# Optimization experiments

Measured on AMD Instinct MI355X. Metric: run time of the kernel, lower is better.

The kernel has to match this reference:

```python
import jax, jax.numpy as jnp
import numpy as np

B, T, D, H = 4, 1024, 1024, 16
DH = D // H
EPS = 1e-5


def setup_inputs() -> dict:
    key = jax.random.key(0)
    ks = jax.random.split(key, 14)
    sc = 1.0 / np.sqrt(D)
    x = jax.random.normal(ks[0], (B, T, D), jnp.float32)
    W_r = jax.random.normal(ks[1], (D, D), jnp.float32) * sc
    W_k = jax.random.normal(ks[2], (D, D), jnp.float32) * sc
    W_v = jax.random.normal(ks[3], (D, D), jnp.float32) * sc
    W_w = jax.random.normal(ks[4], (D, D), jnp.float32) * sc
    W_o = jax.random.normal(ks[5], (D, D), jnp.float32) * sc
    u = jax.random.normal(ks[6], (H, DH), jnp.float32) * 0.1
    tm_r = jax.random.uniform(ks[7], (D,), jnp.float32)
    tm_k = jax.random.uniform(ks[8], (D,), jnp.float32)
    tm_v = jax.random.uniform(ks[9], (D,), jnp.float32)
    tm_w = jax.random.uniform(ks[10], (D,), jnp.float32)
    ln_w = jnp.ones((DH,), jnp.float32) + 0.1 * jax.random.normal(ks[11], (DH,), jnp.float32)
    ln_b = 0.1 * jax.random.normal(ks[12], (DH,), jnp.float32)
    return {"x": x, "W_r": W_r, "W_k": W_k, "W_v": W_v, "W_w": W_w, "W_o": W_o,
            "u": u, "tm_r": tm_r, "tm_k": tm_k, "tm_v": tm_v, "tm_w": tm_w,
            "ln_w": ln_w, "ln_b": ln_b}


def _rwkv6(x, W_r, W_k, W_v, W_w, W_o, u, tm_r, tm_k, tm_v, tm_w, ln_w, ln_b):
    b, t, d = x.shape
    # token-shift mix
    x_prev = jnp.concatenate([jnp.zeros_like(x[:, :1]), x[:, :-1]], axis=1)
    xr = tm_r * x + (1.0 - tm_r) * x_prev
    xk = tm_k * x + (1.0 - tm_k) * x_prev
    xv = tm_v * x + (1.0 - tm_v) * x_prev
    xw = tm_w * x + (1.0 - tm_w) * x_prev
    r = jax.nn.sigmoid(xr @ W_r.T)          # (B,T,D)
    k = xk @ W_k.T
    v = xv @ W_v.T
    w = -jax.nn.softplus(-(xw @ W_w.T)) - 1e-4  # always < 0 -> exp(w) in (0,1)
    r = r.reshape(b, t, H, DH)
    k = k.reshape(b, t, H, DH)
    v = v.reshape(b, t, H, DH)
    w = w.reshape(b, t, H, DH)

    def step(s, rkvw):
        r_t, k_t, v_t, w_t = rkvw  # each (B,H,DH)
        bonus = jnp.exp(u + k_t)[..., :, None] * v_t[..., None, :]  # (B,H,DH,DH)
        o_t = jnp.einsum('bhi,bhij->bhj', r_t, s + bonus)
        s = jnp.exp(w_t)[..., None] * s + k_t[..., :, None] * v_t[..., None, :]
        return s, o_t

    s0 = jnp.zeros((b, H, DH, DH), x.dtype)
    rkvw = tuple(a.transpose(1, 0, 2, 3) for a in (r, k, v, w))  # (T,B,H,DH)
    _, o = jax.lax.scan(step, s0, rkvw)      # o: (T,B,H,DH)
    o = o.transpose(1, 0, 2, 3)              # (B,T,H,DH)
    # group LayerNorm over head dim
    mu = jnp.mean(o, axis=-1, keepdims=True)
    var = jnp.var(o, axis=-1, keepdims=True)
    o = (o - mu) * jax.lax.rsqrt(var + EPS) * ln_w + ln_b
    o = o * r
    return (o.reshape(b, t, d)) @ W_o.T


def reference(x, W_r, W_k, W_v, W_w, W_o, u, tm_r, tm_k, tm_v, tm_w, ln_w, ln_b):
    return _rwkv6(x, W_r, W_k, W_v, W_w, W_o, u, tm_r, tm_k, tm_v, tm_w, ln_w, ln_b)
```

## Files before the change

### kernel.cpp

```cpp
#include <hip/hip_runtime.h>


typedef unsigned short u16;
typedef unsigned int   u32;

typedef __attribute__((ext_vector_type(8))) __bf16 bf16x8;
typedef __attribute__((ext_vector_type(4))) float   f32x4;

#define MB (1u << 20)

#define LDS_PTR(p) ((__attribute__((address_space(3))) void*)(p))
#define GLB_PTR(p) ((const __attribute__((address_space(1))) void*)(p))

__device__ __forceinline__ u16 f2bf(float f) {
  u32 u = __builtin_bit_cast(u32, f);
  u += 0x7FFFu + ((u >> 16) & 1u);
  return (u16)(u >> 16);
}
__device__ __forceinline__ float bf2f(u16 x) {
  u32 u = ((u32)x) << 16;
  return __builtin_bit_cast(float, u);
}
__device__ __forceinline__ u32 pack2(float a, float b) {
  return (u32)f2bf(a) | ((u32)f2bf(b) << 16);
}

__global__ __launch_bounds__(256) void prep_w(
    const float* __restrict__ w0, const float* __restrict__ w1,
    const float* __restrict__ w2, const float* __restrict__ w3,
    const float* __restrict__ w4, u32* __restrict__ out) {
  int idx = blockIdx.x * 256 + threadIdx.x;
  int m = idx >> 19;
  int l = idx & 524287;
  const float* src = (m == 0) ? w0 : (m == 1) ? w1 : (m == 2) ? w2 : (m == 3) ? w3 : w4;
  float2 v = *(const float2*)(src + (size_t)l * 2);
  out[idx] = pack2(v.x, v.y);
}

__global__ __launch_bounds__(256) void prep_mix(
    const float* __restrict__ x,
    const float* __restrict__ tmr, const float* __restrict__ tmk,
    const float* __restrict__ tmv, const float* __restrict__ tmw,
    u32* __restrict__ xr, u32* __restrict__ xk,
    u32* __restrict__ xv, u32* __restrict__ xw) {
  int idx = blockIdx.x * 256 + threadIdx.x;
  int t  = (idx >> 9) & 1023;
  int d0 = (idx & 511) * 2;
  size_t e = (size_t)idx * 2;
  float2 xc = *(const float2*)(x + e);
  float2 xp = make_float2(0.f, 0.f);
  if (t > 0) xp = *(const float2*)(x + e - 1024);
  float2 tm;
  tm = *(const float2*)(tmr + d0);
  xr[idx] = pack2(tm.x * xc.x + (1.f - tm.x) * xp.x, tm.y * xc.y + (1.f - tm.y) * xp.y);
  tm = *(const float2*)(tmk + d0);
  xk[idx] = pack2(tm.x * xc.x + (1.f - tm.x) * xp.x, tm.y * xc.y + (1.f - tm.y) * xp.y);
  tm = *(const float2*)(tmv + d0);
  xv[idx] = pack2(tm.x * xc.x + (1.f - tm.x) * xp.x, tm.y * xc.y + (1.f - tm.y) * xp.y);
  tm = *(const float2*)(tmw + d0);
  xw[idx] = pack2(tm.x * xc.x + (1.f - tm.x) * xp.x, tm.y * xc.y + (1.f - tm.y) * xp.y);
}

__global__ __launch_bounds__(512, 1) void gemm_proj(
    const u16* __restrict__ xr, const u16* __restrict__ xk,
    const u16* __restrict__ xv, const u16* __restrict__ xw,
    const u16* __restrict__ Wr, const u16* __restrict__ Wk,
    const u16* __restrict__ Wv, const u16* __restrict__ Ww,
    u16* __restrict__ rO, u16* __restrict__ kO,
    u16* __restrict__ vO, float* __restrict__ wO) {
  constexpr int KITER = 32;
  constexpr int LDK   = 1024;
  __shared__ __align__(16) u16 Asm[2 * 8192];
  __shared__ __align__(16) u16 Bsm[2 * 8192];

  int mat = blockIdx.z;
  const u16* A = (mat == 0) ? xr : (mat == 1) ? xk : (mat == 2) ? xv : xw;
  const u16* W = (mat == 0) ? Wr : (mat == 1) ? Wk : (mat == 2) ? Wv : Ww;

  int tid = threadIdx.x;
  int m0 = blockIdx.x * 256, n0 = blockIdx.y * 256;
  int wave = tid >> 6, lane = tid & 63;
  int wm = (wave >> 2) * 128;
  int wn = (wave & 3) * 64;
  int r16 = lane & 15, quad = lane >> 4;

  f32x4 acc[8][4] = {};

  int srow0 = wave * 32 + (lane >> 2);
  int srow1 = srow0 + 16;
  int c4    = lane & 3;
  int q0 = c4 ^ ((srow0 >> 1) & 3);
  int q1 = c4 ^ ((srow1 >> 1) & 3);
  const u16* Ag0 = A + (size_t)(m0 + srow0) * LDK + q0 * 8;
  const u16* Ag1 = A + (size_t)(m0 + srow1) * LDK + q1 * 8;
  const u16* Bg0 = W + (size_t)(n0 + srow0) * LDK + q0 * 8;
  const u16* Bg1 = W + (size_t)(n0 + srow1) * LDK + q1 * 8;
  int ldsOff0 = wave * 1024;
  int ldsOff1 = wave * 1024 + 512;

  int aoff[8], boff[4];
#pragma unroll
  for (int mt = 0; mt < 8; ++mt) {
    int r = wm + mt * 16 + r16;
    aoff[mt] = r * 32 + (quad ^ ((r >> 1) & 3)) * 8;
  }
#pragma unroll
  for (int nt = 0; nt < 4; ++nt) {
    int r = wn + nt * 16 + r16;
    boff[nt] = r * 32 + (quad ^ ((r >> 1) & 3)) * 8;
  }

#define ISSUE_TILE(t, buf)                                                              \
  do {                                                                                  \
    int _o = (buf) * 8192, _k = (t) * 32;                                               \
    __builtin_amdgcn_global_load_lds(GLB_PTR(Ag0 + _k), LDS_PTR(Asm + _o + ldsOff0), 16, 0, 0); \
    __builtin_amdgcn_global_load_lds(GLB_PTR(Ag1 + _k), LDS_PTR(Asm + _o + ldsOff1), 16, 0, 0); \
    __builtin_amdgcn_global_load_lds(GLB_PTR(Bg0 + _k), LDS_PTR(Bsm + _o + ldsOff0), 16, 0, 0); \
    __builtin_amdgcn_global_load_lds(GLB_PTR(Bg1 + _k), LDS_PTR(Bsm + _o + ldsOff1), 16, 0, 0); \
  } while (0)

  ISSUE_TILE(0, 0);
  ISSUE_TILE(1, 1);

  int cur = 0;
  for (int i = 0; i < KITER; ++i) {
    if (i < KITER - 1) asm volatile("s_waitcnt vmcnt(4)" ::: "memory");
    else               asm volatile("s_waitcnt vmcnt(0)" ::: "memory");
    __builtin_amdgcn_s_barrier();

    const u16* As = Asm + cur * 8192;
    const u16* Bs = Bsm + cur * 8192;
    bf16x8 af[8], bfm[4];
#pragma unroll
    for (int mt = 0; mt < 8; ++mt) af[mt] = *(const bf16x8*)&As[aoff[mt]];
#pragma unroll
    for (int nt = 0; nt < 4; ++nt) bfm[nt] = *(const bf16x8*)&Bs[boff[nt]];
#pragma unroll
    for (int mt = 0; mt < 8; ++mt)
#pragma unroll
      for (int nt = 0; nt < 4; ++nt)
        acc[mt][nt] = __builtin_amdgcn_mfma_f32_16x16x32_bf16(af[mt], bfm[nt], acc[mt][nt], 0, 0, 0);

    asm volatile("s_waitcnt lgkmcnt(0)" ::: "memory");
    __builtin_amdgcn_s_barrier();
    if (i + 2 < KITER) ISSUE_TILE(i + 2, cur);
    cur ^= 1;
  }
#undef ISSUE_TILE

#pragma unroll
  for (int mt = 0; mt < 8; ++mt) {
#pragma unroll
    for (int nt = 0; nt < 4; ++nt) {
#pragma unroll
      for (int rg = 0; rg < 4; ++rg) {
        int row = m0 + wm + mt * 16 + quad * 4 + rg;
        int col = n0 + wn + nt * 16 + r16;
        float v = acc[mt][nt][rg];
        size_t idx = (size_t)row * 1024 + col;
        if (mat == 0)      rO[idx] = f2bf(1.f / (1.f + __expf(-v)));
        else if (mat == 1) kO[idx] = f2bf(v);
        else if (mat == 2) vO[idx] = f2bf(v);
        else               wO[idx] = v;
      }
    }
  }
}

template <int KITER>
__device__ __forceinline__ void gemm_core(
    const u16* __restrict__ A, const u16* __restrict__ W, float* __restrict__ O,
    u16* Asm, u16* Bsm) {
  constexpr int LDK = KITER * 32;
  int tid = threadIdx.x;
  int m0 = blockIdx.x * 128, n0 = blockIdx.y * 128;
  int wave = tid >> 6, lane = tid & 63;
  int wm = (wave >> 1) * 64, wn = (wave & 1) * 64;
  int r16 = lane & 15, quad = lane >> 4;

  f32x4 acc[4][4] = {};

  int srow0 = wave * 32 + (lane >> 2);
  int srow1 = srow0 + 16;
  int c4    = lane & 3;
  int q0 = c4 ^ ((srow0 >> 1) & 3);
  int q1 = c4 ^ ((srow1 >> 1) & 3);
  const u16* Ag0 = A + (size_t)(m0 + srow0) * LDK + q0 * 8;
  const u16* Ag1 = A + (size_t)(m0 + srow1) * LDK + q1 * 8;
  const u16* Bg0 = W + (size_t)(n0 + srow0) * LDK + q0 * 8;
  const u16* Bg1 = W + (size_t)(n0 + srow1) * LDK + q1 * 8;
  int ldsOff0 = wave * 1024;
  int ldsOff1 = wave * 1024 + 512;

  int aoff[4], boff[4];
#pragma unroll
  for (int mt = 0; mt < 4; ++mt) {
    int r = wm + mt * 16 + r16;
    aoff[mt] = r * 32 + (quad ^ ((r >> 1) & 3)) * 8;
  }
#pragma unroll
  for (int nt = 0; nt < 4; ++nt) {
    int r = wn + nt * 16 + r16;
    boff[nt] = r * 32 + (quad ^ ((r >> 1) & 3)) * 8;
  }

#define ISSUE_TILE(t, buf)                                                              \
  do {                                                                                  \
    int _o = (buf) * 4096, _k = (t) * 32;                                               \
    __builtin_amdgcn_global_load_lds(GLB_PTR(Ag0 + _k), LDS_PTR(Asm + _o + ldsOff0), 16, 0, 0); \
    __builtin_amdgcn_global_load_lds(GLB_PTR(Ag1 + _k), LDS_PTR(Asm + _o + ldsOff1), 16, 0, 0); \
    __builtin_amdgcn_global_load_lds(GLB_PTR(Bg0 + _k), LDS_PTR(Bsm + _o + ldsOff0), 16, 0, 0); \
    __builtin_amdgcn_global_load_lds(GLB_PTR(Bg1 + _k), LDS_PTR(Bsm + _o + ldsOff1), 16, 0, 0); \
  } while (0)

  ISSUE_TILE(0, 0);
  ISSUE_TILE(1, 1);
  ISSUE_TILE(2, 2);

  int cur = 0;
  for (int i = 0; i < KITER; ++i) {
    if (i < KITER - 2)       asm volatile("s_waitcnt vmcnt(8)" ::: "memory");
    else if (i == KITER - 2) asm volatile("s_waitcnt vmcnt(4)" ::: "memory");
    else                     asm volatile("s_waitcnt vmcnt(0)" ::: "memory");
    __builtin_amdgcn_s_barrier();

    const u16* As = Asm + cur * 4096;
    const u16* Bs = Bsm + cur * 4096;
    bf16x8 af[4], bfm[4];
#pragma unroll
    for (int mt = 0; mt < 4; ++mt) af[mt] = *(const bf16x8*)&As[aoff[mt]];
#pragma unroll
    for (int nt = 0; nt < 4; ++nt) bfm[nt] = *(const bf16x8*)&Bs[boff[nt]];
#pragma unroll
    for (int mt = 0; mt < 4; ++mt)
#pragma unroll
      for (int nt = 0; nt < 4; ++nt)
        acc[mt][nt] = __builtin_amdgcn_mfma_f32_16x16x32_bf16(af[mt], bfm[nt], acc[mt][nt], 0, 0, 0);

    asm volatile("s_waitcnt lgkmcnt(0)" ::: "memory");
    __builtin_amdgcn_s_barrier();
    if (i + 3 < KITER) ISSUE_TILE(i + 3, cur);
    cur = (cur == 2) ? 0 : cur + 1;
  }
#undef ISSUE_TILE

#pragma unroll
  for (int mt = 0; mt < 4; ++mt)
#pragma unroll
    for (int nt = 0; nt < 4; ++nt)
#pragma unroll
      for (int rg = 0; rg < 4; ++rg) {
        int row = m0 + wm + mt * 16 + quad * 4 + rg;
        int col = n0 + wn + nt * 16 + r16;
        O[(size_t)row * 1024 + col] = acc[mt][nt][rg];
      }
}

__global__ __launch_bounds__(256) void gemm_out(
    const u16* __restrict__ A, const u16* __restrict__ W, float* __restrict__ O) {
  __shared__ __align__(16) u16 Asm[3 * 4096];
  __shared__ __align__(16) u16 Bsm[3 * 4096];
  gemm_core<32>(A, W, O, Asm, Bsm);
}

__global__ __launch_bounds__(256) void scan_intra(
    const u16* __restrict__ rb, const u16* __restrict__ kb,
    const u16* __restrict__ vb, const float* __restrict__ wb,
    const float* __restrict__ u,
    float* __restrict__ o, u16* __restrict__ rd,
    float* __restrict__ U, float* __restrict__ Dc) {
  int c = blockIdx.x, bh = blockIdx.y;
  int b = bh >> 4, h = bh & 15;
  int tid = threadIdx.x, ig = tid >> 6, j = tid & 63;

  __shared__ __align__(16) float4 combo[4][64];
  __shared__ float vs_[4][64];
  __shared__ float part[4][4][64];

  const float EW_SCALE = 0.99990001f;

  float s[16];
#pragma unroll
  for (int ii = 0; ii < 16; ++ii) s[ii] = 0.f;

  size_t base = ((size_t)(b * 1024 + c * 64)) * 1024 + h * 64 + j;
  float dloc = 1.0f;
  float uval = (ig == 1) ? u[h * 64 + j] : 0.f;

#pragma unroll
  for (int p = 0; p < 2; ++p) {
    size_t idx = base + (size_t)p * 1024;
    if (ig == 0)      combo[p][j].x = bf2f(rb[idx]);
    else if (ig == 1) { float kv = bf2f(kb[idx]); combo[p][j].y = kv; combo[p][j].z = __expf(uval + kv); }
    else if (ig == 2) vs_[p][j] = bf2f(vb[idx]);
    else              combo[p][j].w = EW_SCALE / (1.f + __expf(-wb[idx]));
  }
  __syncthreads();

  for (int tt = 0; tt < 64; tt += 2) {
    if (tt + 2 < 64) {
#pragma unroll
      for (int p = 0; p < 2; ++p) {
        int t2 = tt + 2 + p, sl = t2 & 3;
        size_t idx = base + (size_t)t2 * 1024;
        if (ig == 0)      combo[sl][j].x = bf2f(rb[idx]);
        else if (ig == 1) { float kv = bf2f(kb[idx]); combo[sl][j].y = kv; combo[sl][j].z = __expf(uval + kv); }
        else if (ig == 2) vs_[sl][j] = bf2f(vb[idx]);
        else              combo[sl][j].w = EW_SCALE / (1.f + __expf(-wb[idx]));
      }
    }
#pragma unroll
    for (int p = 0; p < 2; ++p) {
      int t = tt + p, sl = t & 3;
      float vj = vs_[sl][j];
      float acc = 0.f;
#pragma unroll
      for (int ii = 0; ii < 16; ++ii) {
        float4 cb = combo[sl][ig * 16 + ii];
        float tmp = fmaf(cb.z, vj, s[ii]);
        acc = fmaf(cb.x, tmp, acc);
        s[ii] = fmaf(cb.w, s[ii], cb.y * vj);
      }
      part[sl][ig][j] = acc;
      if (ig == 0) {
        rd[base + (size_t)t * 1024] = f2bf(combo[sl][j].x * dloc);
        dloc *= combo[sl][j].w;
      }
    }
    if (tt >= 2) {
      if (ig == 2) {
        int t = tt - 2, sl = t & 3;
        o[base + (size_t)t * 1024] =
            part[sl][0][j] + part[sl][1][j] + part[sl][2][j] + part[sl][3][j];
      } else if (ig == 3) {
        int t = tt - 1, sl = t & 3;
        o[base + (size_t)t * 1024] =
            part[sl][0][j] + part[sl][1][j] + part[sl][2][j] + part[sl][3][j];
      }
    }
    __syncthreads();
  }
  if (ig == 2) {
    o[base + (size_t)62 * 1024] = part[2][0][j] + part[2][1][j] + part[2][2][j] + part[2][3][j];
  } else if (ig == 3) {
    o[base + (size_t)63 * 1024] = part[3][0][j] + part[3][1][j] + part[3][2][j] + part[3][3][j];
  }

  float* Ug = U + (size_t)(bh * 16 + c) * 4096;
#pragma unroll
  for (int ii = 0; ii < 16; ++ii) Ug[(ig * 16 + ii) * 64 + j] = s[ii];
  if (ig == 0) Dc[(bh * 16 + c) * 64 + j] = dloc;
}

__global__ __launch_bounds__(256) void state_prop(
    float* __restrict__ U, const float* __restrict__ Dc) {
  int bh  = blockIdx.x >> 4;
  int e   = (blockIdx.x & 15) * 256 + threadIdx.x;
  int i   = e >> 6;
  float acc = 0.f;
  for (int c = 0; c < 16; ++c) {
    float* Ug = U + (size_t)(bh * 16 + c) * 4096 + e;
    float d = Dc[(bh * 16 + c) * 64 + i];
    float uv = *Ug;
    *Ug = acc;
    acc = fmaf(d, acc, uv);
  }
}

__global__ __launch_bounds__(256) void inter_ln(
    const float* __restrict__ o, const u16* __restrict__ rd,
    const u16* __restrict__ rb, const float* __restrict__ U,
    const float* __restrict__ lnw, const float* __restrict__ lnb,
    u16* __restrict__ oh) {
  int c = blockIdx.x, bh = blockIdx.y;
  int b = bh >> 4, h = bh & 15;
  int tid = threadIdx.x, wave = tid >> 6, lane = tid & 63;
  int l15 = lane & 15, quad = lane >> 4;

  __shared__ __align__(16) u16 Sb[64][72];

  const float* Sg = U + (size_t)(bh * 16 + c) * 4096;
#pragma unroll
  for (int q = 0; q < 16; ++q) {
    int e = q * 256 + tid;
    Sb[e & 63][e >> 6] = f2bf(Sg[e]);
  }
  __syncthreads();

  size_t rbase = ((size_t)(b * 1024 + c * 64)) * 1024 + h * 64;

  const u16* rdg = rd + rbase + (size_t)(wave * 16 + l15) * 1024 + quad * 8;
  bf16x8 af0 = *(const bf16x8*)(rdg);
  bf16x8 af1 = *(const bf16x8*)(rdg + 32);

  f32x4 acc[4] = {};
#pragma unroll
  for (int nt = 0; nt < 4; ++nt) {
    const u16* bp = &Sb[nt * 16 + l15][quad * 8];
    bf16x8 b0 = *(const bf16x8*)bp;
    bf16x8 b1 = *(const bf16x8*)(bp + 32);
    acc[nt] = __builtin_amdgcn_mfma_f32_16x16x32_bf16(af0, b0, acc[nt], 0, 0, 0);
    acc[nt] = __builtin_amdgcn_mfma_f32_16x16x32_bf16(af1, b1, acc[nt], 0, 0, 0);
  }

#pragma unroll
  for (int rg = 0; rg < 4; ++rg) {
    int t = wave * 16 + quad * 4 + rg;
    size_t rowb = rbase + (size_t)t * 1024;
    float v[4];
    float s1 = 0.f, s2 = 0.f;
#pragma unroll
    for (int nt = 0; nt < 4; ++nt) {
      v[nt] = acc[nt][rg] + o[rowb + nt * 16 + l15];
      s1 += v[nt];
      s2 += v[nt] * v[nt];
    }
#pragma unroll
    for (int m = 1; m < 16; m <<= 1) {
      s1 += __shfl_xor(s1, m, 64);
      s2 += __shfl_xor(s2, m, 64);
    }
    float mu  = s1 * (1.f / 64.f);
    float var = s2 * (1.f / 64.f) - mu * mu;
    float rstd = rsqrtf(var + 1e-5f);
#pragma unroll
    for (int nt = 0; nt < 4; ++nt) {
      int jj = nt * 16 + l15;
      float nv = (v[nt] - mu) * rstd;
      float val = (nv * lnw[jj] + lnb[jj]) * bf2f(rb[rowb + jj]);
      oh[rowb + jj] = f2bf(val);
    }
  }
}

extern "C" void kernel_launch(void* const* d_in, const int* in_sizes, int n_in,
                              void* d_out, int out_size, void* d_ws, size_t ws_size,
                              hipStream_t stream) {
  const float* x    = (const float*)d_in[0];
  const float* W_r  = (const float*)d_in[1];
  const float* W_k  = (const float*)d_in[2];
  const float* W_v  = (const float*)d_in[3];
  const float* W_w  = (const float*)d_in[4];
  const float* W_o  = (const float*)d_in[5];
  const float* u    = (const float*)d_in[6];
  const float* tm_r = (const float*)d_in[7];
  const float* tm_k = (const float*)d_in[8];
  const float* tm_v = (const float*)d_in[9];
  const float* tm_w = (const float*)d_in[10];
  const float* ln_w = (const float*)d_in[11];
  const float* ln_b = (const float*)d_in[12];
  float* out = (float*)d_out;

  char* ws = (char*)d_ws;
  u16* xr = (u16*)(ws + (size_t)0 * MB);
  u16* xk = (u16*)(ws + (size_t)8 * MB);
  u16* xv = (u16*)(ws + (size_t)16 * MB);
  u16* xw = (u16*)(ws + (size_t)24 * MB);
  u16* Wb = (u16*)(ws + (size_t)32 * MB);
  u16* Wrb = Wb;
  u16* Wkb = (u16*)(ws + (size_t)34 * MB);
  u16* Wvb = (u16*)(ws + (size_t)36 * MB);
  u16* Wwb = (u16*)(ws + (size_t)38 * MB);
  u16* Wob = (u16*)(ws + (size_t)40 * MB);
  u16*   rbuf = (u16*)(ws + (size_t)48 * MB);
  u16*   kbuf = (u16*)(ws + (size_t)56 * MB);
  u16*   vbuf = (u16*)(ws + (size_t)64 * MB);
  float* wbuf = (float*)(ws + (size_t)72 * MB);
  float* obuf = (float*)(ws + (size_t)88 * MB);
  u16*  rdbuf = (u16*)(ws + (size_t)104 * MB);
  float* Ubuf  = (float*)(ws + (size_t)112 * MB);
  float* Dcbuf = (float*)(ws + (size_t)128 * MB);
  u16*   ohbuf = (u16*)(ws + (size_t)129 * MB);

  prep_w<<<10240, 256, 0, stream>>>(W_r, W_k, W_v, W_w, W_o, (u32*)Wb);
  prep_mix<<<8192, 256, 0, stream>>>(x, tm_r, tm_k, tm_v, tm_w,
                                     (u32*)xr, (u32*)xk, (u32*)xv, (u32*)xw);
  gemm_proj<<<dim3(16, 4, 4), 512, 0, stream>>>(xr, xk, xv, xw,
                                                Wrb, Wkb, Wvb, Wwb,
                                                rbuf, kbuf, vbuf, wbuf);
  scan_intra<<<dim3(16, 64), 256, 0, stream>>>(rbuf, kbuf, vbuf, wbuf, u,
                                               obuf, rdbuf, Ubuf, Dcbuf);
  state_prop<<<1024, 256, 0, stream>>>(Ubuf, Dcbuf);
  inter_ln<<<dim3(16, 64), 256, 0, stream>>>(obuf, rdbuf, rbuf, Ubuf,
                                             ln_w, ln_b, ohbuf);
  gemm_out<<<dim3(32, 8, 1), 256, 0, stream>>>(ohbuf, Wob, out);
}
```

Baseline: 263.9 us.

## Halve scan chunk length to 32 tokens and double chunk-level parallelism

The chunked RWKV scan now uses 32-token chunks instead of 64, doubling the number of scan_intra and inter_ln blocks (2048 instead of 1024) and the length of the serial state_prop loop. This shortens the sequential per-block recurrence and raises occupancy on the many CUs. In exchange the U/Dc state buffers double in size and state_prop does twice as many serial steps. Staging is reworked so two thread groups each load r, k and w together and write one float4, and the U/Dc buffers move into reused workspace regions.

```diff
diff --git a/kernel.cpp b/kernel.cpp
--- a/kernel.cpp
+++ b/kernel.cpp
@@ -283,31 +283,32 @@
 #pragma unroll
   for (int ii = 0; ii < 16; ++ii) s[ii] = 0.f;
 
-  size_t base = ((size_t)(b * 1024 + c * 64)) * 1024 + h * 64 + j;
+  size_t base = ((size_t)(b * 1024 + c * 32)) * 1024 + h * 64 + j;
   float dloc = 1.0f;
-  float uval = (ig == 1) ? u[h * 64 + j] : 0.f;
-
-#pragma unroll
-  for (int p = 0; p < 2; ++p) {
-    size_t idx = base + (size_t)p * 1024;
-    if (ig == 0)      combo[p][j].x = bf2f(rb[idx]);
-    else if (ig == 1) { float kv = bf2f(kb[idx]); combo[p][j].y = kv; combo[p][j].z = __expf(uval + kv); }
-    else if (ig == 2) vs_[p][j] = bf2f(vb[idx]);
-    else              combo[p][j].w = EW_SCALE / (1.f + __expf(-wb[idx]));
-  }
+  float uval = (ig < 2) ? u[h * 64 + j] : 0.f;
+
+#define STAGE(t2, sl)                                                     \
+  do {                                                                    \
+    size_t _idx = base + (size_t)(t2) * 1024;                             \
+    if (ig < 2) {                                                         \
+      float _r = bf2f(rb[_idx]);                                          \
+      float _k = bf2f(kb[_idx]);                                          \
+      float _z = wb[_idx];                                                \
+      combo[sl][j] = make_float4(_r, _k, __expf(uval + _k),               \
+                                 EW_SCALE / (1.f + __expf(-_z)));         \
+    } else {                                                              \
+      vs_[sl][j] = bf2f(vb[_idx]);                                        \
+    }                                                                     \
+  } while (0)
+
+  { int p = ig & 1; STAGE(p, p); }
   __syncthreads();
 
-  for (int tt = 0; tt < 64; tt += 2) {
-    if (tt + 2 < 64) {
-#pragma unroll
-      for (int p = 0; p < 2; ++p) {
-        int t2 = tt + 2 + p, sl = t2 & 3;
-        size_t idx = base + (size_t)t2 * 1024;
-        if (ig == 0)      combo[sl][j].x = bf2f(rb[idx]);
-        else if (ig == 1) { float kv = bf2f(kb[idx]); combo[sl][j].y = kv; combo[sl][j].z = __expf(uval + kv); }
-        else if (ig == 2) vs_[sl][j] = bf2f(vb[idx]);
-        else              combo[sl][j].w = EW_SCALE / (1.f + __expf(-wb[idx]));
-      }
+  for (int tt = 0; tt < 32; tt += 2) {
+    if (tt + 2 < 32) {
+      int p = ig & 1;
+      int t2 = tt + 2 + p;
+      STAGE(t2, t2 & 3);
     }
 #pragma unroll
     for (int p = 0; p < 2; ++p) {
@@ -323,8 +324,9 @@
       }
       part[sl][ig][j] = acc;
       if (ig == 0) {
-        rd[base + (size_t)t * 1024] = f2bf(combo[sl][j].x * dloc);
-        dloc *= combo[sl][j].w;
+        float4 me = combo[sl][j];
+        rd[base + (size_t)t * 1024] = f2bf(me.x * dloc);
+        dloc *= me.w;
       }
     }
     if (tt >= 2) {
@@ -340,16 +342,17 @@
     }
     __syncthreads();
   }
+#undef STAGE
   if (ig == 2) {
-    o[base + (size_t)62 * 1024] = part[2][0][j] + part[2][1][j] + part[2][2][j] + part[2][3][j];
+    o[base + (size_t)30 * 1024] = part[2][0][j] + part[2][1][j] + part[2][2][j] + part[2][3][j];
   } else if (ig == 3) {
-    o[base + (size_t)63 * 1024] = part[3][0][j] + part[3][1][j] + part[3][2][j] + part[3][3][j];
-  }
-
-  float* Ug = U + (size_t)(bh * 16 + c) * 4096;
+    o[base + (size_t)31 * 1024] = part[3][0][j] + part[3][1][j] + part[3][2][j] + part[3][3][j];
+  }
+
+  float* Ug = U + (size_t)(bh * 32 + c) * 4096;
 #pragma unroll
   for (int ii = 0; ii < 16; ++ii) Ug[(ig * 16 + ii) * 64 + j] = s[ii];
-  if (ig == 0) Dc[(bh * 16 + c) * 64 + j] = dloc;
+  if (ig == 0) Dc[(bh * 32 + c) * 64 + j] = dloc;
 }
 
 __global__ __launch_bounds__(256) void state_prop(
@@ -358,16 +361,16 @@
   int e   = (blockIdx.x & 15) * 256 + threadIdx.x;
   int i   = e >> 6;
   float acc = 0.f;
-  for (int c = 0; c < 16; ++c) {
-    float* Ug = U + (size_t)(bh * 16 + c) * 4096 + e;
-    float d = Dc[(bh * 16 + c) * 64 + i];
+  for (int c = 0; c < 32; ++c) {
+    float* Ug = U + (size_t)(bh * 32 + c) * 4096 + e;
+    float d = Dc[(bh * 32 + c) * 64 + i];
     float uv = *Ug;
     *Ug = acc;
     acc = fmaf(d, acc, uv);
   }
 }
 
-__global__ __launch_bounds__(256) void inter_ln(
+__global__ __launch_bounds__(128) void inter_ln(
     const float* __restrict__ o, const u16* __restrict__ rd,
     const u16* __restrict__ rb, const float* __restrict__ U,
     const float* __restrict__ lnw, const float* __restrict__ lnb,
@@ -379,15 +382,15 @@
 
   __shared__ __align__(16) u16 Sb[64][72];
 
-  const float* Sg = U + (size_t)(bh * 16 + c) * 4096;
-#pragma unroll
-  for (int q = 0; q < 16; ++q) {
-    int e = q * 256 + tid;
+  const float* Sg = U + (size_t)(bh * 32 + c) * 4096;
+#pragma unroll
+  for (int q = 0; q < 32; ++q) {
+    int e = q * 128 + tid;
     Sb[e & 63][e >> 6] = f2bf(Sg[e]);
   }
   __syncthreads();
 
-  size_t rbase = ((size_t)(b * 1024 + c * 64)) * 1024 + h * 64;
+  size_t rbase = ((size_t)(b * 1024 + c * 32)) * 1024 + h * 64;
 
   const u16* rdg = rd + rbase + (size_t)(wave * 16 + l15) * 1024 + quad * 8;
   bf16x8 af0 = *(const bf16x8*)(rdg);
@@ -456,20 +459,20 @@
   u16* xk = (u16*)(ws + (size_t)8 * MB);
   u16* xv = (u16*)(ws + (size_t)16 * MB);
   u16* xw = (u16*)(ws + (size_t)24 * MB);
+  float* Ubuf = (float*)(ws + (size_t)0 * MB);
   u16* Wb = (u16*)(ws + (size_t)32 * MB);
   u16* Wrb = Wb;
   u16* Wkb = (u16*)(ws + (size_t)34 * MB);
   u16* Wvb = (u16*)(ws + (size_t)36 * MB);
   u16* Wwb = (u16*)(ws + (size_t)38 * MB);
   u16* Wob = (u16*)(ws + (size_t)40 * MB);
+  float* Dcbuf = (float*)(ws + (size_t)42 * MB);
   u16*   rbuf = (u16*)(ws + (size_t)48 * MB);
   u16*   kbuf = (u16*)(ws + (size_t)56 * MB);
   u16*   vbuf = (u16*)(ws + (size_t)64 * MB);
   float* wbuf = (float*)(ws + (size_t)72 * MB);
   float* obuf = (float*)(ws + (size_t)88 * MB);
   u16*  rdbuf = (u16*)(ws + (size_t)104 * MB);
-  float* Ubuf  = (float*)(ws + (size_t)112 * MB);
-  float* Dcbuf = (float*)(ws + (size_t)128 * MB);
   u16*   ohbuf = (u16*)(ws + (size_t)129 * MB);
 
   prep_w<<<10240, 256, 0, stream>>>(W_r, W_k, W_v, W_w, W_o, (u32*)Wb);
@@ -478,10 +481,10 @@
   gemm_proj<<<dim3(16, 4, 4), 512, 0, stream>>>(xr, xk, xv, xw,
                                                 Wrb, Wkb, Wvb, Wwb,
                                                 rbuf, kbuf, vbuf, wbuf);
-  scan_intra<<<dim3(16, 64), 256, 0, stream>>>(rbuf, kbuf, vbuf, wbuf, u,
+  scan_intra<<<dim3(32, 64), 256, 0, stream>>>(rbuf, kbuf, vbuf, wbuf, u,
                                                obuf, rdbuf, Ubuf, Dcbuf);
   state_prop<<<1024, 256, 0, stream>>>(Ubuf, Dcbuf);
-  inter_ln<<<dim3(16, 64), 256, 0, stream>>>(obuf, rdbuf, rbuf, Ubuf,
+  inter_ln<<<dim3(32, 64), 128, 0, stream>>>(obuf, rdbuf, rbuf, Ubuf,
                                              ln_w, ln_b, ohbuf);
   gemm_out<<<dim3(32, 8, 1), 256, 0, stream>>>(ohbuf, Wob, out);
 }
```

Result: no change. 265.2 us (+0.5%).
